# Optimization experiments

Measured on AMD Instinct MI355X. Metric: run time of the kernel, lower is better.

Reference implementation:

```python
import math
import jax, jax.numpy as jnp
import numpy as np

B, L, C, H = 8, 1024, 1024, 16
D = C // H  # head_dim = 64
MAX_SCALE_MUL = math.log(100.0)


def setup_inputs() -> dict:
    key = jax.random.key(0)
    ks = jax.random.split(key, 8)
    x = jax.random.normal(ks[0], (B, L, C), dtype=jnp.float32)
    # rotary frequencies: angle(l, j) = l * theta^(-2j/D), stored as (cos, sin)
    theta = 10000.0
    inv_freq = theta ** (-jnp.arange(0, D, 2, dtype=jnp.float32) / D)  # [D/2]
    ang = jnp.arange(L, dtype=jnp.float32)[:, None] * inv_freq[None, :]  # [L, D/2]
    freqs_cis = jnp.stack([jnp.cos(ang), jnp.sin(ang)], axis=-1)  # [L, D/2, 2]
    attn_bias = jnp.zeros((1, 1, L, L), dtype=jnp.float32)
    W_qkv = jax.random.normal(ks[1], (3 * C, C), dtype=jnp.float32) * (1.0 / math.sqrt(C))
    q_bias = jnp.zeros((C,), dtype=jnp.float32)
    v_bias = jnp.zeros((C,), dtype=jnp.float32)
    scale_mul_log = jnp.full((1, H, 1, 1), math.log(4.0), dtype=jnp.float32)
    W_proj = jax.random.normal(ks[2], (C, C), dtype=jnp.float32) * (1.0 / math.sqrt(C))
    b_proj = jnp.zeros((C,), dtype=jnp.float32)
    return {"x": x, "freqs_cis": freqs_cis, "attn_bias": attn_bias,
            "W_qkv": W_qkv, "q_bias": q_bias, "v_bias": v_bias,
            "scale_mul_log": scale_mul_log, "W_proj": W_proj, "b_proj": b_proj}


def _l2norm(t):
    # F.normalize(t, dim=-1): t / max(||t||_2, eps)
    n = jnp.sqrt(jnp.sum(t * t, axis=-1, keepdims=True))
    return t / jnp.maximum(n, 1e-12)


def _rope(t, fr):
    # t: [B,H,L,D]; fr: [L,D/2,2] (cos,sin). Complex mul on adjacent pairs.
    b, h, l, d = t.shape
    t2 = t.reshape(b, h, l, d // 2, 2)
    c = fr[None, None, :, :, 0]
    s = fr[None, None, :, :, 1]
    re = t2[..., 0] * c - t2[..., 1] * s
    im = t2[..., 0] * s + t2[..., 1] * c
    return jnp.stack([re, im], axis=-1).reshape(b, h, l, d)


def reference(x, freqs_cis, attn_bias, W_qkv, q_bias, v_bias, scale_mul_log, W_proj, b_proj):
    b, l, c = x.shape
    bias = jnp.concatenate([q_bias, jnp.zeros_like(q_bias), v_bias])  # [3C]
    qkv = (x @ W_qkv.T + bias).reshape(b, l, 3, H, D)
    # permute(2,0,3,1,4) -> q,k,v each [B,H,L,D]
    q = jnp.transpose(qkv[:, :, 0], (0, 2, 1, 3))
    k = jnp.transpose(qkv[:, :, 1], (0, 2, 1, 3))
    v = jnp.transpose(qkv[:, :, 2], (0, 2, 1, 3))
    # attn_l2_norm path: learned per-head scale, softmax scale = 1
    scale_mul = jnp.exp(jnp.minimum(scale_mul_log, MAX_SCALE_MUL))  # [1,H,1,1]
    q = _l2norm(q) * scale_mul
    k = _l2norm(k)
    q = _rope(q, freqs_cis)
    k = _rope(k, freqs_cis)
    scores = jnp.einsum('bhqd,bhkd->bhqk', q, k) * 1.0 + attn_bias
    attn = jax.nn.softmax(scores, axis=-1)
    out = jnp.einsum('bhqk,bhkd->bhqd', attn, v)
    out = jnp.transpose(out, (0, 2, 1, 3)).reshape(b, l, c)
    return out @ W_proj.T + b_proj
```

## Files before the change

kernel.cpp:

```cpp
#include <hip/hip_runtime.h>
#include <math.h>

#define PB 8
#define PL 1024
#define PC 1024
#define PH 16
#define PD 64
#define MAX_SCALE_MUL 4.605170185988092f
#define LOG2E 1.4426950408889634f

typedef __attribute__((ext_vector_type(8))) short s16x8;
typedef __attribute__((ext_vector_type(4))) float f32x4;

#define MFMA16(a, b, c) __builtin_amdgcn_mfma_f32_16x16x32_bf16(a, b, c, 0, 0, 0)

#if __has_builtin(__builtin_amdgcn_exp2f)
#define EXP2(x) __builtin_amdgcn_exp2f(x)
#else
#define EXP2(x) exp2f(x)
#endif

__device__ __forceinline__ unsigned short f2bf(float f) {
    unsigned u = __float_as_uint(f);
    unsigned r = (u + 0x7fffu + ((u >> 16) & 1u)) >> 16;
    return (unsigned short)r;
}

__device__ __forceinline__ unsigned pk2bf(float a, float b) {
#if __has_builtin(__builtin_amdgcn_cvt_pk_bf16_f32)
    typedef __attribute__((ext_vector_type(2))) __bf16 bf16x2_t;
    bf16x2_t r = __builtin_amdgcn_cvt_pk_bf16_f32(a, b);
    return __builtin_bit_cast(unsigned, r);
#else
    return (unsigned)f2bf(a) | ((unsigned)f2bf(b) << 16);
#endif
}

__device__ __forceinline__ void gl2lds16(const void* g, void* l) {
    __builtin_amdgcn_global_load_lds(
        (const __attribute__((address_space(1))) unsigned int*)g,
        (__attribute__((address_space(3))) unsigned int*)l, 16, 0, 0);
}

__global__ __launch_bounds__(256) void cast3f_kernel(
    const float* __restrict__ a, const float* __restrict__ b,
    const float* __restrict__ c, const float* __restrict__ bias,
    unsigned short* __restrict__ oa, unsigned short* __restrict__ ob,
    unsigned short* __restrict__ oc, int* __restrict__ flag)
{
    int blk = blockIdx.x;
    if (blk >= 12288) {
        int idx = (blk - 12288) * 256 + threadIdx.x;
        const float4* b4 = (const float4*)bias;
        bool nz = false;
#pragma unroll
        for (int i = 0; i < 4; i++) {
            float4 v = b4[idx * 4 + i];
            nz |= (v.x != 0.f) | (v.y != 0.f) | (v.z != 0.f) | (v.w != 0.f);
        }
        if (nz) atomicOr(flag, 1);
        return;
    }
    const float* src; unsigned short* dst; int base;
    if (blk < 8192)       { src = a; dst = oa; base = blk; }
    else if (blk < 11264) { src = b; dst = ob; base = blk - 8192; }
    else                  { src = c; dst = oc; base = blk - 11264; }
    int i = base * 256 + threadIdx.x;
    float4 v = ((const float4*)src)[i];
    ((uint2*)dst)[i] = make_uint2(pk2bf(v.x, v.y), pk2bf(v.z, v.w));
}

template<int VMODE>
__global__ __launch_bounds__(256) void gemm_qkv_lean(
    const unsigned short* __restrict__ Xh,
    const unsigned short* __restrict__ Wh,
    const float* __restrict__ qb, const float* __restrict__ vb,
    const float* __restrict__ freqs,
    unsigned short* __restrict__ Qh, unsigned short* __restrict__ Kh,
    unsigned short* __restrict__ Vt)
{
    __shared__ unsigned short As[128 * 64];
    __shared__ unsigned short Bs[128 * 64];
    const int tid  = threadIdx.x;
    const int wave = tid >> 6, lane = tid & 63;
    const int wm = wave & 1, wn = wave >> 1;
    const int quad = lane >> 4, rr = lane & 15;

    const int nwg    = gridDim.x * gridDim.y;
    const int lin    = blockIdx.y * gridDim.x + blockIdx.x;
    const int newlin = (lin & 7) * (nwg >> 3) + (lin >> 3);
    const int m0 = (newlin & 63) * 128;
    const int n0 = ((newlin >> 6) + (VMODE ? 16 : 0)) * 128;

    f32x4 acc[4][4];
#pragma unroll
    for (int i = 0; i < 4; i++)
#pragma unroll
        for (int j = 0; j < 4; j++) acc[i][j] = (f32x4){0.f, 0.f, 0.f, 0.f};

    const int r8 = lane >> 3;
    const int c8 = lane & 7;
    const int g  = c8 ^ r8;
    const unsigned short* gA = Xh + (size_t)(m0 + wave * 32 + r8) * 1024 + g * 8;
    const unsigned short* gB = Wh + (size_t)(n0 + wave * 32 + r8) * 1024 + g * 8;
    unsigned short* lA = &As[(wave * 32) * 64];
    unsigned short* lB = &Bs[(wave * 32) * 64];

    const int swz8 = rr & 7;

    for (int k0 = 0; k0 < 16; k0++) {
#pragma unroll
        for (int t = 0; t < 4; t++) {
            gl2lds16(gA + (size_t)t * 8192, &lA[(t * 8) * 64]);
            gl2lds16(gB + (size_t)t * 8192, &lB[(t * 8) * 64]);
        }
        gA += 64; gB += 64;
        __syncthreads();

#pragma unroll
        for (int kk = 0; kk < 2; kk++) {
            const int coff = ((kk * 4 + quad) ^ swz8) * 8;
            s16x8 wf[4], xf[4];
#pragma unroll
            for (int i = 0; i < 4; i++)
                wf[i] = *(const s16x8*)&Bs[(wn * 64 + i * 16 + rr) * 64 + coff];
#pragma unroll
            for (int j = 0; j < 4; j++)
                xf[j] = *(const s16x8*)&As[(wm * 64 + j * 16 + rr) * 64 + coff];
            if constexpr (VMODE == 0) {
#pragma unroll
                for (int i = 0; i < 4; i++)
#pragma unroll
                    for (int j = 0; j < 4; j++)
                        acc[i][j] = MFMA16(wf[i], xf[j], acc[i][j]);
            } else {
#pragma unroll
                for (int i = 0; i < 4; i++)
#pragma unroll
                    for (int j = 0; j < 4; j++)
                        acc[i][j] = MFMA16(xf[j], wf[i], acc[i][j]);
            }
        }
        __syncthreads();
    }

    const int b   = m0 >> 10;
    const int h   = ((n0 & 1023) + wn * 64) >> 6;
    const int lb0 = (m0 & 1023) + wm * 64;

    if constexpr (VMODE) {
        unsigned short* basep = Vt + (size_t)(b * PH + h) * PD * PL;
#pragma unroll
        for (int i = 0; i < 4; i++) {
            const int d = i * 16 + rr;
            const float bv = vb[h * 64 + d];
#pragma unroll
            for (int j = 0; j < 4; j++) {
                const int l0 = lb0 + j * 16 + quad * 4;
                uint2 pk = make_uint2(pk2bf(acc[i][j][0] + bv, acc[i][j][1] + bv),
                                      pk2bf(acc[i][j][2] + bv, acc[i][j][3] + bv));
                *(uint2*)(basep + (size_t)d * PL + l0) = pk;
            }
        }
    } else {
        const int which = n0 >> 10;
        if (which == 0) {
            unsigned short* basep = Qh + (size_t)(b * PH + h) * PL * PD;
#pragma unroll
            for (int i = 0; i < 4; i++) {
                const int d0 = i * 16 + quad * 4;
                const float4 b4 = *(const float4*)(qb + h * 64 + d0);
#pragma unroll
                for (int j = 0; j < 4; j++) {
                    const int l = lb0 + j * 16 + rr;
                    uint2 pk = make_uint2(
                        pk2bf(acc[i][j][0] + b4.x, acc[i][j][1] + b4.y),
                        pk2bf(acc[i][j][2] + b4.z, acc[i][j][3] + b4.w));
                    *(uint2*)(basep + (size_t)l * PD + d0) = pk;
                }
            }
        } else {
            unsigned short* basep = Kh + (size_t)(b * PH + h) * PL * PD;
            const float2* fr2 = (const float2*)freqs;
#pragma unroll
            for (int j = 0; j < 4; j++) {
                float ss = 0.f;
#pragma unroll
                for (int i = 0; i < 4; i++)
                    ss = fmaf(acc[i][j][0], acc[i][j][0],
                         fmaf(acc[i][j][1], acc[i][j][1],
                         fmaf(acc[i][j][2], acc[i][j][2],
                         fmaf(acc[i][j][3], acc[i][j][3], ss))));
                ss += __shfl_xor(ss, 16);
                ss += __shfl_xor(ss, 32);
                const float scale = 1.0f / fmaxf(sqrtf(ss), 1e-12f);
                const int l = lb0 + j * 16 + rr;
#pragma unroll
                for (int i = 0; i < 4; i++) {
                    const int d0 = i * 16 + quad * 4;
                    const float2 cs0 = fr2[(size_t)l * 32 + (d0 >> 1)];
                    const float2 cs1 = fr2[(size_t)l * 32 + (d0 >> 1) + 1];
                    const float a0 = acc[i][j][0] * scale, a1 = acc[i][j][1] * scale;
                    const float a2 = acc[i][j][2] * scale, a3 = acc[i][j][3] * scale;
                    uint2 pk = make_uint2(
                        pk2bf(a0 * cs0.x - a1 * cs0.y, fmaf(a0, cs0.y, a1 * cs0.x)),
                        pk2bf(a2 * cs1.x - a3 * cs1.y, fmaf(a2, cs1.y, a3 * cs1.x)));
                    *(uint2*)(basep + (size_t)l * PD + d0) = pk;
                }
            }
        }
    }
}

__global__ __launch_bounds__(256, 4) void attn_mfma(
    const unsigned short* __restrict__ Qh, const unsigned short* __restrict__ Kh,
    const unsigned short* __restrict__ Vt, const float* __restrict__ bias,
    const float* __restrict__ sml, const int* __restrict__ biasflag,
    const float* __restrict__ freqs, unsigned short* __restrict__ O)
{
    __shared__ unsigned short Ks[2][64 * 64];
    __shared__ unsigned short Vs[2][64 * 64];
    __shared__ unsigned int   Ps[4][16 * 32];

    const int tid  = threadIdx.x;
    const int wave = tid >> 6, lane = tid & 63;
    const int quad = lane >> 4, rr = lane & 15;

    const int lin = blockIdx.y * 128 + blockIdx.x;
    const int j   = lin >> 3;
    const int bh  = ((lin & 7) << 4) | (j & 15);
    const int q0  = (j >> 4) * 128;

    const int b = bh >> 4, h = bh & 15;
    const int hasbias = *biasflag;

    const float M = __expf(fminf(sml[h], MAX_SCALE_MUL)) * LOG2E;
    const f32x4 negM = (f32x4){-M, -M, -M, -M};

    const int sr = wave * 16 + (lane >> 3);
    const int sc = lane & 7;
    const int sg = sc ^ (sr & 7);
    const int swz8 = rr & 7;
    const int psw  = (rr & 7) << 2;

    const size_t kvbase = (size_t)bh * PL * PD;
    const float2* fr2 = (const float2*)freqs;

    auto stage = [&](int buf, int kb) {
        gl2lds16(Kh + kvbase + (size_t)(kb * 64 + sr) * PD + sg * 8,
                 &Ks[buf][(wave * 16) * 64]);
        gl2lds16(Kh + kvbase + (size_t)(kb * 64 + sr + 8) * PD + sg * 8,
                 &Ks[buf][(wave * 16 + 8) * 64]);
        gl2lds16(Vt + kvbase + (size_t)sr * PL + kb * 64 + sg * 8,
                 &Vs[buf][(wave * 16) * 64]);
        gl2lds16(Vt + kvbase + (size_t)(sr + 8) * PL + kb * 64 + sg * 8,
                 &Vs[buf][(wave * 16 + 8) * 64]);
    };

    stage(0, 0);

    s16x8 qB[2][2];
#pragma unroll
    for (int g = 0; g < 2; g++) {
        const int ql = q0 + g * 64 + wave * 16 + rr;
        const size_t qoff = ((size_t)bh * PL + ql) * PD;
        uint4 r0 = *(const uint4*)(Qh + qoff + quad * 8);
        uint4 r1 = *(const uint4*)(Qh + qoff + 32 + quad * 8);
        unsigned uu[8] = {r0.x, r0.y, r0.z, r0.w, r1.x, r1.y, r1.z, r1.w};
        float ss = 0.f;
#pragma unroll
        for (int m = 0; m < 8; m++) {
            float lo = __uint_as_float(uu[m] << 16);
            float hi = __uint_as_float(uu[m] & 0xffff0000u);
            ss = fmaf(lo, lo, fmaf(hi, hi, ss));
        }
        ss += __shfl_xor(ss, 16);
        ss += __shfl_xor(ss, 32);
        const float scale = M / fmaxf(sqrtf(ss), 1e-12f);
        unsigned outw[8];
#pragma unroll
        for (int m = 0; m < 8; m++) {
            const int idx = (m >> 2) * 16 + quad * 4 + (m & 3);
            float2 cs = fr2[(size_t)ql * 32 + idx];
            float lo = __uint_as_float(uu[m] << 16);
            float hi = __uint_as_float(uu[m] & 0xffff0000u);
            float av = lo * scale, bv = hi * scale;
            outw[m] = pk2bf(av * cs.x - bv * cs.y, fmaf(av, cs.y, bv * cs.x));
        }
        qB[g][0] = __builtin_bit_cast(s16x8, make_uint4(outw[0], outw[1], outw[2], outw[3]));
        qB[g][1] = __builtin_bit_cast(s16x8, make_uint4(outw[4], outw[5], outw[6], outw[7]));
    }

    f32x4 accO[2][4];
#pragma unroll
    for (int g = 0; g < 2; g++)
#pragma unroll
        for (int jd = 0; jd < 4; jd++) accO[g][jd] = (f32x4){0.f, 0.f, 0.f, 0.f};
    float lsum[2] = {0.f, 0.f};

    __syncthreads();

    int cur = 0;
    for (int kb = 0; kb < 16; kb++) {
        if (kb < 15) stage(cur ^ 1, kb + 1);

        unsigned ps[2][4][2];
#pragma unroll
        for (int s = 0; s < 4; s++) {
            const s16x8 k0 = *(const s16x8*)&Ks[cur][(s * 16 + rr) * 64 + ((0 + quad) ^ swz8) * 8];
            const s16x8 k1 = *(const s16x8*)&Ks[cur][(s * 16 + rr) * 64 + ((4 + quad) ^ swz8) * 8];
#pragma unroll
            for (int g = 0; g < 2; g++) {
                __builtin_amdgcn_s_setprio(1);
                f32x4 z = MFMA16(k0, qB[g][0], negM);
                z = MFMA16(k1, qB[g][1], z);
                __builtin_amdgcn_s_setprio(0);
                if (hasbias) {
                    const float* brow = bias + (size_t)(q0 + g * 64 + wave * 16 + rr) * PL + kb * 64;
                    float4 bv = *(const float4*)(brow + s * 16 + quad * 4);
                    z[0] = fmaf(bv.x, LOG2E, z[0]);
                    z[1] = fmaf(bv.y, LOG2E, z[1]);
                    z[2] = fmaf(bv.z, LOG2E, z[2]);
                    z[3] = fmaf(bv.w, LOG2E, z[3]);
                }
                z[0] = EXP2(z[0]); z[1] = EXP2(z[1]);
                z[2] = EXP2(z[2]); z[3] = EXP2(z[3]);
                lsum[g] += (z[0] + z[1]) + (z[2] + z[3]);
                ps[g][s][0] = pk2bf(z[0], z[1]);
                ps[g][s][1] = pk2bf(z[2], z[3]);
            }
        }

        s16x8 pB[2][2];
#pragma unroll
        for (int g = 0; g < 2; g++) {
#pragma unroll
            for (int s = 0; s < 4; s++)
                *(uint2*)&Ps[wave][rr * 32 + ((s * 8 + quad * 2) ^ psw)] =
                    make_uint2(ps[g][s][0], ps[g][s][1]);
            pB[g][0] = *(const s16x8*)&Ps[wave][rr * 32 + ((quad * 4) ^ psw)];
            pB[g][1] = *(const s16x8*)&Ps[wave][rr * 32 + ((16 + quad * 4) ^ psw)];
        }
#pragma unroll
        for (int jd = 0; jd < 4; jd++) {
            const s16x8 v0 = *(const s16x8*)&Vs[cur][(jd * 16 + rr) * 64 + ((0 + quad) ^ swz8) * 8];
            const s16x8 v1 = *(const s16x8*)&Vs[cur][(jd * 16 + rr) * 64 + ((4 + quad) ^ swz8) * 8];
            __builtin_amdgcn_s_setprio(1);
#pragma unroll
            for (int g = 0; g < 2; g++) {
                accO[g][jd] = MFMA16(v0, pB[g][0], accO[g][jd]);
                accO[g][jd] = MFMA16(v1, pB[g][1], accO[g][jd]);
            }
            __builtin_amdgcn_s_setprio(0);
        }

        __syncthreads();
        cur ^= 1;
    }

    const int lr = lane >> 2, cch = lane & 3;
    const int pswl = (lr & 7) << 2;
#pragma unroll
    for (int g = 0; g < 2; g++) {
        float ls = lsum[g];
        ls += __shfl_xor(ls, 16);
        ls += __shfl_xor(ls, 32);
        float inv = 1.0f / ls;
#pragma unroll
        for (int jd = 0; jd < 4; jd++) {
            *(uint2*)&Ps[wave][rr * 32 + ((jd * 8 + quad * 2) ^ psw)] =
                make_uint2(pk2bf(accO[g][jd][0] * inv, accO[g][jd][1] * inv),
                           pk2bf(accO[g][jd][2] * inv, accO[g][jd][3] * inv));
        }
        uint4 w0 = *(const uint4*)&Ps[wave][lr * 32 + ((cch * 8) ^ pswl)];
        uint4 w1 = *(const uint4*)&Ps[wave][lr * 32 + ((cch * 8 + 4) ^ pswl)];
        size_t ob = ((size_t)(b * PL + q0 + g * 64 + wave * 16 + lr) * PC + h * PD);
        *(uint4*)(O + ob + cch * 16)     = w0;
        *(uint4*)(O + ob + cch * 16 + 8) = w1;
    }
}

__global__ __launch_bounds__(256) void gemm_proj_mfma(
    const unsigned short* __restrict__ Ah,
    const unsigned short* __restrict__ Wh,
    const float* __restrict__ bp, float* __restrict__ Out)
{
    __shared__ unsigned short As[128 * 64];
    __shared__ unsigned short Bs[128 * 64];
    const int tid  = threadIdx.x;
    const int wave = tid >> 6, lane = tid & 63;
    const int wm = wave & 1, wn = wave >> 1;
    const int quad = lane >> 4, rr = lane & 15;

    const int nwg    = gridDim.x * gridDim.y;
    const int lin    = blockIdx.y * gridDim.x + blockIdx.x;
    const int newlin = (lin & 7) * (nwg >> 3) + (lin >> 3);
    const int m0 = (newlin & 63) * 128;
    const int n0 = (newlin >> 6) * 128;

    f32x4 acc[4][4];
#pragma unroll
    for (int i = 0; i < 4; i++)
#pragma unroll
        for (int j = 0; j < 4; j++) acc[i][j] = (f32x4){0.f, 0.f, 0.f, 0.f};

    const int r8 = lane >> 3;
    const int c8 = lane & 7;
    const int g  = c8 ^ r8;
    const unsigned short* gA = Ah + (size_t)(m0 + wave * 32 + r8) * 1024 + g * 8;
    const unsigned short* gB = Wh + (size_t)(n0 + wave * 32 + r8) * 1024 + g * 8;
    unsigned short* lA = &As[(wave * 32) * 64];
    unsigned short* lB = &Bs[(wave * 32) * 64];

    const int swz8 = rr & 7;

    for (int k0 = 0; k0 < 16; k0++) {
#pragma unroll
        for (int t = 0; t < 4; t++) {
            gl2lds16(gA + (size_t)t * 8192, &lA[(t * 8) * 64]);
            gl2lds16(gB + (size_t)t * 8192, &lB[(t * 8) * 64]);
        }
        gA += 64; gB += 64;
        __syncthreads();

#pragma unroll
        for (int kk = 0; kk < 2; kk++) {
            const int coff = ((kk * 4 + quad) ^ swz8) * 8;
            s16x8 wf[4], xf[4];
#pragma unroll
            for (int i = 0; i < 4; i++)
                wf[i] = *(const s16x8*)&Bs[(wn * 64 + i * 16 + rr) * 64 + coff];
#pragma unroll
            for (int j = 0; j < 4; j++)
                xf[j] = *(const s16x8*)&As[(wm * 64 + j * 16 + rr) * 64 + coff];
#pragma unroll
            for (int i = 0; i < 4; i++)
#pragma unroll
                for (int j = 0; j < 4; j++)
                    acc[i][j] = MFMA16(wf[i], xf[j], acc[i][j]);
        }
        __syncthreads();
    }

#pragma unroll
    for (int i = 0; i < 4; i++) {
        const int nn = n0 + wn * 64 + i * 16 + quad * 4;
        const float4 bb = *(const float4*)(bp + nn);
#pragma unroll
        for (int j = 0; j < 4; j++) {
            const int m = m0 + wm * 64 + j * 16 + rr;
            float4 o = make_float4(acc[i][j][0] + bb.x, acc[i][j][1] + bb.y,
                                   acc[i][j][2] + bb.z, acc[i][j][3] + bb.w);
            *(float4*)(Out + (size_t)m * 1024 + nn) = o;
        }
    }
}

extern "C" void kernel_launch(void* const* d_in, const int* in_sizes, int n_in,
                              void* d_out, int out_size, void* d_ws, size_t ws_size,
                              hipStream_t stream)
{
    const float* x         = (const float*)d_in[0];
    const float* freqs     = (const float*)d_in[1];
    const float* attn_bias = (const float*)d_in[2];
    const float* W_qkv     = (const float*)d_in[3];
    const float* q_bias    = (const float*)d_in[4];
    const float* v_bias    = (const float*)d_in[5];
    const float* sml       = (const float*)d_in[6];
    const float* W_proj    = (const float*)d_in[7];
    const float* b_proj    = (const float*)d_in[8];
    float* out = (float*)d_out;

    unsigned char* w = (unsigned char*)d_ws;
    const size_t MB = 1ull << 20;
    unsigned short* xh  = (unsigned short*)(w + 0);
    unsigned short* wqh = (unsigned short*)(w + 16 * MB);
    unsigned short* wph = (unsigned short*)(w + 22 * MB);
    unsigned short* Qh  = (unsigned short*)(w + 24 * MB);
    unsigned short* Kh  = (unsigned short*)(w + 40 * MB);
    unsigned short* Vt  = (unsigned short*)(w + 72 * MB);
    unsigned short* Oh  = (unsigned short*)(w + 88 * MB);
    int*            flg = (int*)(w + 104 * MB);

    hipMemsetAsync(flg, 0, sizeof(int), stream);
    cast3f_kernel<<<12544, 256, 0, stream>>>(x, W_qkv, W_proj, attn_bias,
                                             xh, wqh, wph, flg);
    gemm_qkv_lean<0><<<dim3(64, 16), 256, 0, stream>>>(
        xh, wqh, q_bias, v_bias, freqs, Qh, Kh, Vt);
    gemm_qkv_lean<1><<<dim3(64, 8), 256, 0, stream>>>(
        xh, wqh, q_bias, v_bias, freqs, Qh, Kh, Vt);
    attn_mfma<<<dim3(128, 8), 256, 0, stream>>>(Qh, Kh, Vt, attn_bias, sml, flg, freqs, Oh);
    gemm_proj_mfma<<<dim3(64, 8), 256, 0, stream>>>(Oh, wph, b_proj, out);
}
```

Measured before the change: 270.0 us.

## Merge QKV GEMM launches, template attention on bias flag, drop block swizzles

```diff
diff --git a/kernel.cpp b/kernel.cpp
--- a/kernel.cpp
+++ b/kernel.cpp
@@ -1,5 +1,6 @@
 #include <hip/hip_runtime.h>
 #include <math.h>
+#include <type_traits>
 
 #define PB 8
 #define PL 1024
@@ -70,7 +71,6 @@
     ((uint2*)dst)[i] = make_uint2(pk2bf(v.x, v.y), pk2bf(v.z, v.w));
 }
 
-template<int VMODE>
 __global__ __launch_bounds__(256) void gemm_qkv_lean(
     const unsigned short* __restrict__ Xh,
     const unsigned short* __restrict__ Wh,
@@ -85,12 +85,9 @@
     const int wave = tid >> 6, lane = tid & 63;
     const int wm = wave & 1, wn = wave >> 1;
     const int quad = lane >> 4, rr = lane & 15;
-
-    const int nwg    = gridDim.x * gridDim.y;
-    const int lin    = blockIdx.y * gridDim.x + blockIdx.x;
-    const int newlin = (lin & 7) * (nwg >> 3) + (lin >> 3);
-    const int m0 = (newlin & 63) * 128;
-    const int n0 = ((newlin >> 6) + (VMODE ? 16 : 0)) * 128;
+    const int m0 = blockIdx.x * 128;
+    const int n0 = blockIdx.y * 128;
+    const bool vmode = (n0 >= 2048);
 
     f32x4 acc[4][4];
 #pragma unroll
@@ -108,47 +105,52 @@
 
     const int swz8 = rr & 7;
 
-    for (int k0 = 0; k0 < 16; k0++) {
-#pragma unroll
-        for (int t = 0; t < 4; t++) {
-            gl2lds16(gA + (size_t)t * 8192, &lA[(t * 8) * 64]);
-            gl2lds16(gB + (size_t)t * 8192, &lB[(t * 8) * 64]);
-        }
-        gA += 64; gB += 64;
-        __syncthreads();
-
-#pragma unroll
-        for (int kk = 0; kk < 2; kk++) {
-            const int coff = ((kk * 4 + quad) ^ swz8) * 8;
-            s16x8 wf[4], xf[4];
-#pragma unroll
-            for (int i = 0; i < 4; i++)
-                wf[i] = *(const s16x8*)&Bs[(wn * 64 + i * 16 + rr) * 64 + coff];
-#pragma unroll
-            for (int j = 0; j < 4; j++)
-                xf[j] = *(const s16x8*)&As[(wm * 64 + j * 16 + rr) * 64 + coff];
-            if constexpr (VMODE == 0) {
+    auto kloop = [&](auto vm) {
+        constexpr int VM = decltype(vm)::value;
+        for (int k0 = 0; k0 < 16; k0++) {
+#pragma unroll
+            for (int t = 0; t < 4; t++) {
+                gl2lds16(gA + (size_t)t * 8192, &lA[(t * 8) * 64]);
+                gl2lds16(gB + (size_t)t * 8192, &lB[(t * 8) * 64]);
+            }
+            gA += 64; gB += 64;
+            __syncthreads();
+
+#pragma unroll
+            for (int kk = 0; kk < 2; kk++) {
+                const int coff = ((kk * 4 + quad) ^ swz8) * 8;
+                s16x8 wf[4], xf[4];
 #pragma unroll
                 for (int i = 0; i < 4; i++)
-#pragma unroll
-                    for (int j = 0; j < 4; j++)
-                        acc[i][j] = MFMA16(wf[i], xf[j], acc[i][j]);
-            } else {
-#pragma unroll
-                for (int i = 0; i < 4; i++)
-#pragma unroll
-                    for (int j = 0; j < 4; j++)
-                        acc[i][j] = MFMA16(xf[j], wf[i], acc[i][j]);
-            }
-        }
-        __syncthreads();
-    }
+                    wf[i] = *(const s16x8*)&Bs[(wn * 64 + i * 16 + rr) * 64 + coff];
+#pragma unroll
+                for (int j = 0; j < 4; j++)
+                    xf[j] = *(const s16x8*)&As[(wm * 64 + j * 16 + rr) * 64 + coff];
+                if constexpr (VM == 0) {
+#pragma unroll
+                    for (int i = 0; i < 4; i++)
+#pragma unroll
+                        for (int j = 0; j < 4; j++)
+                            acc[i][j] = MFMA16(wf[i], xf[j], acc[i][j]);
+                } else {
+#pragma unroll
+                    for (int i = 0; i < 4; i++)
+#pragma unroll
+                        for (int j = 0; j < 4; j++)
+                            acc[i][j] = MFMA16(xf[j], wf[i], acc[i][j]);
+                }
+            }
+            __syncthreads();
+        }
+    };
+    if (vmode) kloop(std::integral_constant<int, 1>{});
+    else       kloop(std::integral_constant<int, 0>{});
 
     const int b   = m0 >> 10;
     const int h   = ((n0 & 1023) + wn * 64) >> 6;
     const int lb0 = (m0 & 1023) + wm * 64;
 
-    if constexpr (VMODE) {
+    if (vmode) {
         unsigned short* basep = Vt + (size_t)(b * PH + h) * PD * PL;
 #pragma unroll
         for (int i = 0; i < 4; i++) {
@@ -225,12 +227,7 @@
     const int tid  = threadIdx.x;
     const int wave = tid >> 6, lane = tid & 63;
     const int quad = lane >> 4, rr = lane & 15;
-
-    const int lin = blockIdx.y * 128 + blockIdx.x;
-    const int j   = lin >> 3;
-    const int bh  = ((lin & 7) << 4) | (j & 15);
-    const int q0  = (j >> 4) * 128;
-
+    const int bh = blockIdx.x, q0 = blockIdx.y * 128;
     const int b = bh >> 4, h = bh & 15;
     const int hasbias = *biasflag;
 
@@ -300,63 +297,68 @@
 
     __syncthreads();
 
-    int cur = 0;
-    for (int kb = 0; kb < 16; kb++) {
-        if (kb < 15) stage(cur ^ 1, kb + 1);
-
-        unsigned ps[2][4][2];
-#pragma unroll
-        for (int s = 0; s < 4; s++) {
-            const s16x8 k0 = *(const s16x8*)&Ks[cur][(s * 16 + rr) * 64 + ((0 + quad) ^ swz8) * 8];
-            const s16x8 k1 = *(const s16x8*)&Ks[cur][(s * 16 + rr) * 64 + ((4 + quad) ^ swz8) * 8];
+    auto kbloop = [&](auto hb) {
+        constexpr int HB = decltype(hb)::value;
+        int cur = 0;
+        for (int kb = 0; kb < 16; kb++) {
+            if (kb < 15) stage(cur ^ 1, kb + 1);
+
+            unsigned ps[2][4][2];
+#pragma unroll
+            for (int s = 0; s < 4; s++) {
+                const s16x8 k0 = *(const s16x8*)&Ks[cur][(s * 16 + rr) * 64 + ((0 + quad) ^ swz8) * 8];
+                const s16x8 k1 = *(const s16x8*)&Ks[cur][(s * 16 + rr) * 64 + ((4 + quad) ^ swz8) * 8];
+#pragma unroll
+                for (int g = 0; g < 2; g++) {
+                    __builtin_amdgcn_s_setprio(1);
+                    f32x4 z = MFMA16(k0, qB[g][0], negM);
+                    z = MFMA16(k1, qB[g][1], z);
+                    __builtin_amdgcn_s_setprio(0);
+                    if constexpr (HB) {
+                        const float* brow = bias + (size_t)(q0 + g * 64 + wave * 16 + rr) * PL + kb * 64;
+                        float4 bv = *(const float4*)(brow + s * 16 + quad * 4);
+                        z[0] = fmaf(bv.x, LOG2E, z[0]);
+                        z[1] = fmaf(bv.y, LOG2E, z[1]);
+                        z[2] = fmaf(bv.z, LOG2E, z[2]);
+                        z[3] = fmaf(bv.w, LOG2E, z[3]);
+                    }
+                    z[0] = EXP2(z[0]); z[1] = EXP2(z[1]);
+                    z[2] = EXP2(z[2]); z[3] = EXP2(z[3]);
+                    lsum[g] += (z[0] + z[1]) + (z[2] + z[3]);
+                    ps[g][s][0] = pk2bf(z[0], z[1]);
+                    ps[g][s][1] = pk2bf(z[2], z[3]);
+                }
+            }
+
+            s16x8 pB[2][2];
 #pragma unroll
             for (int g = 0; g < 2; g++) {
+#pragma unroll
+                for (int s = 0; s < 4; s++)
+                    *(uint2*)&Ps[wave][rr * 32 + ((s * 8 + quad * 2) ^ psw)] =
+                        make_uint2(ps[g][s][0], ps[g][s][1]);
+                pB[g][0] = *(const s16x8*)&Ps[wave][rr * 32 + ((quad * 4) ^ psw)];
+                pB[g][1] = *(const s16x8*)&Ps[wave][rr * 32 + ((16 + quad * 4) ^ psw)];
+            }
+#pragma unroll
+            for (int jd = 0; jd < 4; jd++) {
+                const s16x8 v0 = *(const s16x8*)&Vs[cur][(jd * 16 + rr) * 64 + ((0 + quad) ^ swz8) * 8];
+                const s16x8 v1 = *(const s16x8*)&Vs[cur][(jd * 16 + rr) * 64 + ((4 + quad) ^ swz8) * 8];
                 __builtin_amdgcn_s_setprio(1);
-                f32x4 z = MFMA16(k0, qB[g][0], negM);
-                z = MFMA16(k1, qB[g][1], z);
+#pragma unroll
+                for (int g = 0; g < 2; g++) {
+                    accO[g][jd] = MFMA16(v0, pB[g][0], accO[g][jd]);
+                    accO[g][jd] = MFMA16(v1, pB[g][1], accO[g][jd]);
+                }
                 __builtin_amdgcn_s_setprio(0);
-                if (hasbias) {
-                    const float* brow = bias + (size_t)(q0 + g * 64 + wave * 16 + rr) * PL + kb * 64;
-                    float4 bv = *(const float4*)(brow + s * 16 + quad * 4);
-                    z[0] = fmaf(bv.x, LOG2E, z[0]);
-                    z[1] = fmaf(bv.y, LOG2E, z[1]);
-                    z[2] = fmaf(bv.z, LOG2E, z[2]);
-                    z[3] = fmaf(bv.w, LOG2E, z[3]);
-                }
-                z[0] = EXP2(z[0]); z[1] = EXP2(z[1]);
-                z[2] = EXP2(z[2]); z[3] = EXP2(z[3]);
-                lsum[g] += (z[0] + z[1]) + (z[2] + z[3]);
-                ps[g][s][0] = pk2bf(z[0], z[1]);
-                ps[g][s][1] = pk2bf(z[2], z[3]);
-            }
-        }
-
-        s16x8 pB[2][2];
-#pragma unroll
-        for (int g = 0; g < 2; g++) {
-#pragma unroll
-            for (int s = 0; s < 4; s++)
-                *(uint2*)&Ps[wave][rr * 32 + ((s * 8 + quad * 2) ^ psw)] =
-                    make_uint2(ps[g][s][0], ps[g][s][1]);
-            pB[g][0] = *(const s16x8*)&Ps[wave][rr * 32 + ((quad * 4) ^ psw)];
-            pB[g][1] = *(const s16x8*)&Ps[wave][rr * 32 + ((16 + quad * 4) ^ psw)];
-        }
-#pragma unroll
-        for (int jd = 0; jd < 4; jd++) {
-            const s16x8 v0 = *(const s16x8*)&Vs[cur][(jd * 16 + rr) * 64 + ((0 + quad) ^ swz8) * 8];
-            const s16x8 v1 = *(const s16x8*)&Vs[cur][(jd * 16 + rr) * 64 + ((4 + quad) ^ swz8) * 8];
-            __builtin_amdgcn_s_setprio(1);
-#pragma unroll
-            for (int g = 0; g < 2; g++) {
-                accO[g][jd] = MFMA16(v0, pB[g][0], accO[g][jd]);
-                accO[g][jd] = MFMA16(v1, pB[g][1], accO[g][jd]);
-            }
-            __builtin_amdgcn_s_setprio(0);
-        }
-
-        __syncthreads();
-        cur ^= 1;
-    }
+            }
+
+            __syncthreads();
+            cur ^= 1;
+        }
+    };
+    if (hasbias) kbloop(std::integral_constant<int, 1>{});
+    else         kbloop(std::integral_constant<int, 0>{});
 
     const int lr = lane >> 2, cch = lane & 3;
     const int pswl = (lr & 7) << 2;
@@ -391,12 +393,7 @@
     const int wave = tid >> 6, lane = tid & 63;
     const int wm = wave & 1, wn = wave >> 1;
     const int quad = lane >> 4, rr = lane & 15;
-
-    const int nwg    = gridDim.x * gridDim.y;
-    const int lin    = blockIdx.y * gridDim.x + blockIdx.x;
-    const int newlin = (lin & 7) * (nwg >> 3) + (lin >> 3);
-    const int m0 = (newlin & 63) * 128;
-    const int n0 = (newlin >> 6) * 128;
+    const int m0 = blockIdx.x * 128, n0 = blockIdx.y * 128;
 
     f32x4 acc[4][4];
 #pragma unroll
@@ -485,9 +482,7 @@
     hipMemsetAsync(flg, 0, sizeof(int), stream);
     cast3f_kernel<<<12544, 256, 0, stream>>>(x, W_qkv, W_proj, attn_bias,
                                              xh, wqh, wph, flg);
-    gemm_qkv_lean<0><<<dim3(64, 16), 256, 0, stream>>>(
-        xh, wqh, q_bias, v_bias, freqs, Qh, Kh, Vt);
-    gemm_qkv_lean<1><<<dim3(64, 8), 256, 0, stream>>>(
+    gemm_qkv_lean<<<dim3(64, 24), 256, 0, stream>>>(
         xh, wqh, q_bias, v_bias, freqs, Qh, Kh, Vt);
     attn_mfma<<<dim3(128, 8), 256, 0, stream>>>(Qh, Kh, Vt, attn_bias, sml, flg, freqs, Oh);
     gemm_proj_mfma<<<dim3(64, 8), 256, 0, stream>>>(Oh, wph, b_proj, out);
```

Result: faster. 250.9 us (-7.1%).
